# Kernel tuning notes

Measured on AMD Instinct MI355X. Metric: run time of the kernel, lower is better.

## Reference

```python
import jax, jax.numpy as jnp
import numpy as np

N, E, G = 50000, 600000, 128
ND, ED, H, T, L = 32, 16, 128, 128, 4


def setup_inputs() -> dict:
    key = jax.random.key(0)
    ks = jax.random.split(key, 32)
    s = 0.05
    nrm = lambda k, shp: (jax.random.normal(k, shp, jnp.float32) * s)
    inp = {
        'node_f': jax.random.normal(ks[0], (N, ND), jnp.float32),
        'node_x': jax.random.normal(ks[1], (N, 3), jnp.float32),
        'edge_w': jax.random.normal(ks[2], (E, ED), jnp.float32),
        'src': jax.random.randint(ks[3], (E,), 0, N, jnp.int32),
        'dst': jax.random.randint(ks[4], (E,), 0, N, jnp.int32),
        'graph_ids': jnp.sort(jax.random.randint(ks[5], (N,), 0, G, jnp.int32)),
        'W_in': nrm(ks[6], (ND, H)), 'b_in': jnp.zeros((H,), jnp.float32),
        'W_e': nrm(ks[7], (ED, H)), 'b_e': jnp.zeros((H,), jnp.float32),
        'msg_W1': nrm(ks[8], (L, 3 * H + 1, H)), 'msg_b1': jnp.zeros((L, H), jnp.float32),
        'msg_W2': nrm(ks[9], (L, H, H)), 'msg_b2': jnp.zeros((L, H), jnp.float32),
        'upd_W1': nrm(ks[10], (L, H, H)), 'upd_b1': jnp.zeros((L, H), jnp.float32),
        'upd_W2': nrm(ks[11], (L, H, H)), 'upd_b2': jnp.zeros((L, H), jnp.float32),
        'W_out': nrm(ks[12], (2 * H, T)), 'b_out': jnp.zeros((T,), jnp.float32),
    }
    return inp


def reference(node_f, node_x, edge_w, src, dst, graph_ids,
              W_in, b_in, W_e, b_e,
              msg_W1, msg_b1, msg_W2, msg_b2,
              upd_W1, upd_b1, upd_W2, upd_b2,
              W_out, b_out):
    relu = jax.nn.relu
    # input node / edge embeddings
    f = relu(node_f @ W_in + b_in)            # [N, H]
    w = relu(edge_w @ W_e + b_e)              # [E, H]
    # squared distance per edge (positions are static across layers)
    sq = jnp.sum((node_x[src] - node_x[dst]) ** 2, axis=-1, keepdims=True)  # [E, 1]
    for i in range(L):
        mi = jnp.concatenate([f[src], f[dst], w, sq], axis=-1)  # [E, 3H+1]
        m = relu(relu(mi @ msg_W1[i] + msg_b1[i]) @ msg_W2[i] + msg_b2[i])  # [E, H]
        m_sum = jax.ops.segment_sum(m, dst, num_segments=N)     # scatter-sum to dst
        u = m_sum + f
        f = relu(relu(u @ upd_W1[i] + upd_b1[i]) @ upd_W2[i] + upd_b2[i])
    # per-graph mean / max readout
    counts = jax.ops.segment_sum(jnp.ones((N,), f.dtype), graph_ids, num_segments=G)
    mean = jax.ops.segment_sum(f, graph_ids, num_segments=G) / jnp.maximum(counts, 1.0)[:, None]
    mx = jax.ops.segment_max(f, graph_ids, num_segments=G)
    mx = jnp.where(counts[:, None] > 0, mx, 0.0)
    return jnp.concatenate([mean, mx], axis=-1) @ W_out + b_out  # [G, T]
```

## Files before the change

kernel.cpp:

```cpp
#include <hip/hip_runtime.h>
#include <hip/hip_fp16.h>

typedef _Float16 f16;
typedef _Float16 f16x8 __attribute__((ext_vector_type(8)));
typedef float f32x4 __attribute__((ext_vector_type(4)));

#define N_NODES 50000
#define N_EDGES 600000
#define G_GRAPHS 128
#define H 128
#define NP 50176
#define NT_E 18750
#define NB_E 1024
#define NT_N 1563

__global__ void k_f0(const float* __restrict__ node_f, const float* __restrict__ W_in,
                     const float* __restrict__ b_in, f16* __restrict__ fh)
{
    __shared__ float sW[32 * 128];
    __shared__ float sx[8][32];
    const int tid = threadIdx.x;
    const int base = blockIdx.x * 8;
    for (int i = tid; i < 32 * 128; i += 128) sW[i] = W_in[i];
    for (int i = tid; i < 8 * 32; i += 128) {
        int u = i >> 5, k = i & 31;
        int n = base + u;
        sx[u][k] = (n < N_NODES) ? node_f[(size_t)n * 32 + k] : 0.0f;
    }
    __syncthreads();
    const float bj = b_in[tid];
    #pragma unroll
    for (int u = 0; u < 8; ++u) {
        int n = base + u;
        if (n >= N_NODES) break;
        float acc = bj;
        #pragma unroll
        for (int k = 0; k < 32; ++k) acc = fmaf(sx[u][k], sW[k * 128 + tid], acc);
        fh[(size_t)n * H + tid] = (f16)fmaxf(acc, 0.0f);
    }
}

__global__ void k_hist(const int* __restrict__ dst, int* __restrict__ cnt)
{
    int e = blockIdx.x * 256 + threadIdx.x;
    if (e < N_EDGES) atomicAdd(&cnt[dst[e]], 1);
}

__global__ void k_scanA(const int* __restrict__ cnt, int* __restrict__ rowptr,
                        int* __restrict__ bsum)
{
    __shared__ int s[256];
    const int t = threadIdx.x;
    const int i = blockIdx.x * 256 + t;
    int v = cnt[i];
    s[t] = v;
    __syncthreads();
    #pragma unroll
    for (int off = 1; off < 256; off <<= 1) {
        int x = (t >= off) ? s[t - off] : 0;
        __syncthreads();
        s[t] += x;
        __syncthreads();
    }
    rowptr[i] = s[t] - v;
    if (t == 255) bsum[blockIdx.x] = s[255];
}

__global__ void k_scanB(const int* __restrict__ bsum, int* __restrict__ boff)
{
    __shared__ int s[256];
    const int t = threadIdx.x;
    int v = (t < 196) ? bsum[t] : 0;
    s[t] = v;
    __syncthreads();
    #pragma unroll
    for (int off = 1; off < 256; off <<= 1) {
        int x = (t >= off) ? s[t - off] : 0;
        __syncthreads();
        s[t] += x;
        __syncthreads();
    }
    boff[t] = s[t] - v;
}

__global__ void k_scanC(int* __restrict__ rowptr, const int* __restrict__ boff)
{
    int i = blockIdx.x * 256 + threadIdx.x;
    rowptr[i] += boff[blockIdx.x];
}

__global__ void k_scatter_idx(const int* __restrict__ dst, const int* __restrict__ rowptr,
                              int* __restrict__ fill, int* __restrict__ perm_eidx)
{
    int e = blockIdx.x * 256 + threadIdx.x;
    if (e >= N_EDGES) return;
    int d = dst[e];
    int p = rowptr[d] + atomicAdd(&fill[d], 1);
    perm_eidx[p] = e;
}

__global__ void k_gather(const int* __restrict__ perm_eidx, const float* __restrict__ edge_w,
                         const int* __restrict__ src, const int* __restrict__ dst,
                         const float* __restrict__ node_x,
                         int* __restrict__ perm_src, int* __restrict__ perm_dst,
                         float* __restrict__ perm_sq, f16* __restrict__ perm_ewh)
{
    int pp = blockIdx.x * 256 + threadIdx.x;
    if (pp >= N_EDGES) return;
    int e = perm_eidx[pp];
    int s = src[e], d = dst[e];
    float dx = node_x[s * 3 + 0] - node_x[d * 3 + 0];
    float dy = node_x[s * 3 + 1] - node_x[d * 3 + 1];
    float dz = node_x[s * 3 + 2] - node_x[d * 3 + 2];
    perm_src[pp] = s;
    perm_dst[pp] = d;
    perm_sq[pp] = dx * dx + dy * dy + dz * dz;
    const float4* pw = (const float4*)(edge_w + (size_t)e * 16);
    float4 w0 = pw[0], w1 = pw[1], w2 = pw[2], w3 = pw[3];
    f16x8 v0, v1;
    v0[0] = (f16)w0.x; v0[1] = (f16)w0.y; v0[2] = (f16)w0.z; v0[3] = (f16)w0.w;
    v0[4] = (f16)w1.x; v0[5] = (f16)w1.y; v0[6] = (f16)w1.z; v0[7] = (f16)w1.w;
    v1[0] = (f16)w2.x; v1[1] = (f16)w2.y; v1[2] = (f16)w2.z; v1[3] = (f16)w2.w;
    v1[4] = (f16)w3.x; v1[5] = (f16)w3.y; v1[6] = (f16)w3.z; v1[7] = (f16)w3.w;
    f16x8* q = (f16x8*)(perm_ewh + (size_t)pp * 16);
    q[0] = v0; q[1] = v1;
}

__global__ __launch_bounds__(512, 2) void k_edge2(
    const f16* __restrict__ fh,
    const int* __restrict__ perm_src, const int* __restrict__ perm_dst,
    const float* __restrict__ perm_sq, const f16* __restrict__ perm_ewh,
    const float* __restrict__ W_e, const float* __restrict__ b_e,
    const float* __restrict__ W1, const float* __restrict__ b1,
    const float* __restrict__ W2, const float* __restrict__ b2,
    f16* __restrict__ msum)
{
    const int tid = threadIdx.x;
    const int wave = tid >> 6;
    const int lane = tid & 63;
    const int l16 = lane & 15;
    const int lq  = lane >> 4;
    const int col = wave * 16 + l16;

    f16x8 wef, w1f[12], w2f[4];
    #pragma unroll
    for (int j = 0; j < 8; ++j) {
        int k = lq * 8 + j;
        wef[j] = (k < 16) ? (f16)W_e[(size_t)k * H + col] : (f16)0.0f;
    }
    #pragma unroll
    for (int k = 0; k < 12; ++k)
        #pragma unroll
        for (int j = 0; j < 8; ++j)
            w1f[k][j] = (f16)W1[(size_t)(k * 32 + lq * 8 + j) * H + col];
    #pragma unroll
    for (int k = 0; k < 4; ++k)
        #pragma unroll
        for (int j = 0; j < 8; ++j)
            w2f[k][j] = (f16)W2[(size_t)(k * 32 + lq * 8 + j) * H + col];
    const float w1last = W1[(size_t)384 * H + col];
    const float b1v = b1[col], b2v = b2[col], bev = b_e[col];

    __shared__ alignas(16) f16 Atile[32][392];
    __shared__ alignas(16) f16 h1B[2][32][136];
    __shared__ int   s_src[2][32];
    __shared__ int   s_dst[2][32];
    __shared__ float s_sq[2][32];

    const int b = ((blockIdx.x & 7) << 7) | (blockIdx.x >> 3);
    const int t0 = (int)((long)b * NT_E / NB_E);
    const int t1 = (int)((long)(b + 1) * NT_E / NB_E);

    if (tid < 32) {
        int e = t0 * 32 + tid;
        s_src[0][tid] = perm_src[e];
        s_dst[0][tid] = perm_dst[e];
        s_sq[0][tid]  = perm_sq[e];
    }
    __syncthreads();

    int p = 0, q = 0;
    for (int t = t0; t < t1; ++t, p ^= 1, q ^= 1) {
        {
            int row = tid >> 4, ch = tid & 15;
            int j = ((row >> 2) & 3) * 8 + (row >> 4) * 4 + (row & 3);
            int sv = s_src[p][j];
            int dv = s_dst[p][j];
            ((int4*)&Atile[row][0])[ch]   = ((const int4*)(fh + (size_t)sv * H))[ch];
            ((int4*)&Atile[row][128])[ch] = ((const int4*)(fh + (size_t)dv * H))[ch];
        }
        #pragma unroll
        for (int m = 0; m < 2; ++m) {
            f16x8 a;
            if (lq < 2) {
                int j = (l16 >> 2) * 8 + m * 4 + (l16 & 3);
                int e = t * 32 + j;
                a = *(const f16x8*)(perm_ewh + (size_t)e * 16 + lq * 8);
            } else {
                #pragma unroll
                for (int jj = 0; jj < 8; ++jj) a[jj] = (f16)0.0f;
            }
            f32x4 c = {bev, bev, bev, bev};
            c = __builtin_amdgcn_mfma_f32_16x16x32_f16(a, wef, c, 0, 0, 0);
            #pragma unroll
            for (int r = 0; r < 4; ++r)
                Atile[m * 16 + lq * 4 + r][256 + col] = (f16)fmaxf(c[r], 0.0f);
        }
        if (tid < 32 && t + 1 < t1) {
            int e = (t + 1) * 32 + tid;
            s_src[p ^ 1][tid] = perm_src[e];
            s_dst[p ^ 1][tid] = perm_dst[e];
            s_sq[p ^ 1][tid]  = perm_sq[e];
        }
        __syncthreads();

        int dc[8];
        f32x4 acc1[2];
        #pragma unroll
        for (int m = 0; m < 2; ++m)
            #pragma unroll
            for (int r = 0; r < 4; ++r) {
                int j = lq * 8 + m * 4 + r;
                dc[m * 4 + r] = s_dst[p][j];
                acc1[m][r] = fmaf(s_sq[p][j], w1last, b1v);
            }
        #pragma unroll
        for (int k = 0; k < 12; ++k) {
            #pragma unroll
            for (int m = 0; m < 2; ++m) {
                f16x8 a = *(const f16x8*)&Atile[m * 16 + l16][k * 32 + lq * 8];
                acc1[m] = __builtin_amdgcn_mfma_f32_16x16x32_f16(a, w1f[k], acc1[m], 0, 0, 0);
            }
        }
        #pragma unroll
        for (int m = 0; m < 2; ++m)
            #pragma unroll
            for (int r = 0; r < 4; ++r)
                h1B[q][m * 16 + lq * 4 + r][col] = (f16)fmaxf(acc1[m][r], 0.0f);
        __syncthreads();

        f32x4 acc2[2];
        #pragma unroll
        for (int m = 0; m < 2; ++m) {
            f32x4 c = {b2v, b2v, b2v, b2v};
            acc2[m] = c;
        }
        #pragma unroll
        for (int k = 0; k < 4; ++k) {
            #pragma unroll
            for (int m = 0; m < 2; ++m) {
                f16x8 a = *(const f16x8*)&h1B[q][m * 16 + l16][k * 32 + lq * 8];
                acc2[m] = __builtin_amdgcn_mfma_f32_16x16x32_f16(a, w2f[k], acc2[m], 0, 0, 0);
            }
        }
        {
            float run = fmaxf(acc2[0][0], 0.0f);
            int cd = dc[0];
            #pragma unroll
            for (int i = 1; i < 8; ++i) {
                float v = fmaxf(acc2[i >> 2][i & 3], 0.0f);
                int d = dc[i];
                if (d == cd) {
                    run += v;
                } else {
                    float nb = __shfl_xor(run, 1);
                    if ((l16 & 1) == 0) {
                        union { f16 h[2]; __half2 v2; } u;
                        u.h[0] = (f16)run; u.h[1] = (f16)nb;
                        unsafeAtomicAdd((__half2*)&msum[(size_t)cd * H + col], u.v2);
                    }
                    run = v; cd = d;
                }
            }
            float nb = __shfl_xor(run, 1);
            if ((l16 & 1) == 0) {
                union { f16 h[2]; __half2 v2; } u;
                u.h[0] = (f16)run; u.h[1] = (f16)nb;
                unsafeAtomicAdd((__half2*)&msum[(size_t)cd * H + col], u.v2);
            }
        }
    }
}

__global__ __launch_bounds__(256, 4) void k_update(
    const f16* __restrict__ msum, f16* __restrict__ fh,
    const float* __restrict__ W1, const float* __restrict__ b1,
    const float* __restrict__ W2, const float* __restrict__ b2)
{
    const int tid = threadIdx.x;
    const int wave = tid >> 6;
    const int lane = tid & 63;
    const int l16 = lane & 15;
    const int lq = lane >> 4;
    const int colbase = wave * 32;

    f16x8 w1fr[4][2], w2fr[4][2];
    float b1v[2], b2v[2];
    #pragma unroll
    for (int nt = 0; nt < 2; ++nt) {
        const int col = colbase + nt * 16 + l16;
        #pragma unroll
        for (int k = 0; k < 4; ++k) {
            f16x8 v1, v2;
            #pragma unroll
            for (int j = 0; j < 8; ++j) {
                v1[j] = (f16)W1[(size_t)(k * 32 + lq * 8 + j) * H + col];
                v2[j] = (f16)W2[(size_t)(k * 32 + lq * 8 + j) * H + col];
            }
            w1fr[k][nt] = v1;
            w2fr[k][nt] = v2;
        }
        b1v[nt] = b1[col];
        b2v[nt] = b2[col];
    }

    __shared__ alignas(16) f16 U[32][136];
    for (int tile = blockIdx.x; tile < NT_N; tile += gridDim.x) {
        __syncthreads();
        const int n0 = tile * 32;
        {
            int row = tid >> 3, ch = tid & 7;
            int n = n0 + row;
            if (n < N_NODES) {
                const f16x8* pm = (const f16x8*)(msum + (size_t)n * H) + ch * 2;
                const f16x8* pf = (const f16x8*)(fh + (size_t)n * H) + ch * 2;
                f16x8 m0 = pm[0], m1 = pm[1];
                f16x8 f0 = pf[0], f1 = pf[1];
                f16 tmp[16];
                #pragma unroll
                for (int j = 0; j < 8; ++j) {
                    tmp[j]     = (f16)((float)m0[j] + (float)f0[j]);
                    tmp[8 + j] = (f16)((float)m1[j] + (float)f1[j]);
                }
                int4* q0 = (int4*)(&U[row][ch * 16]);
                q0[0] = ((const int4*)tmp)[0];
                q0[1] = ((const int4*)tmp)[1];
            }
        }
        __syncthreads();

        f32x4 acc[2][2];
        #pragma unroll
        for (int m = 0; m < 2; ++m)
            #pragma unroll
            for (int nt = 0; nt < 2; ++nt) {
                f32x4 c = {b1v[nt], b1v[nt], b1v[nt], b1v[nt]};
                acc[m][nt] = c;
            }
        #pragma unroll
        for (int k = 0; k < 4; ++k) {
            #pragma unroll
            for (int m = 0; m < 2; ++m) {
                f16x8 a = *(const f16x8*)&U[m * 16 + l16][k * 32 + lq * 8];
                #pragma unroll
                for (int nt = 0; nt < 2; ++nt)
                    acc[m][nt] = __builtin_amdgcn_mfma_f32_16x16x32_f16(a, w1fr[k][nt], acc[m][nt], 0, 0, 0);
            }
        }
        __syncthreads();
        #pragma unroll
        for (int m = 0; m < 2; ++m)
            #pragma unroll
            for (int nt = 0; nt < 2; ++nt)
                #pragma unroll
                for (int r = 0; r < 4; ++r)
                    U[m * 16 + lq * 4 + r][colbase + nt * 16 + l16] = (f16)fmaxf(acc[m][nt][r], 0.0f);
        __syncthreads();

        f32x4 acc2[2][2];
        #pragma unroll
        for (int m = 0; m < 2; ++m)
            #pragma unroll
            for (int nt = 0; nt < 2; ++nt) {
                f32x4 c = {b2v[nt], b2v[nt], b2v[nt], b2v[nt]};
                acc2[m][nt] = c;
            }
        #pragma unroll
        for (int k = 0; k < 4; ++k) {
            #pragma unroll
            for (int m = 0; m < 2; ++m) {
                f16x8 a = *(const f16x8*)&U[m * 16 + l16][k * 32 + lq * 8];
                #pragma unroll
                for (int nt = 0; nt < 2; ++nt)
                    acc2[m][nt] = __builtin_amdgcn_mfma_f32_16x16x32_f16(a, w2fr[k][nt], acc2[m][nt], 0, 0, 0);
            }
        }
        #pragma unroll
        for (int m = 0; m < 2; ++m)
            #pragma unroll
            for (int nt = 0; nt < 2; ++nt)
                #pragma unroll
                for (int r = 0; r < 4; ++r) {
                    int row = m * 16 + lq * 4 + r;
                    int n = n0 + row;
                    if (n < N_NODES)
                        fh[(size_t)n * H + colbase + nt * 16 + l16] = (f16)fmaxf(acc2[m][nt][r], 0.0f);
                }
    }
}

__global__ void k_readout(const f16* __restrict__ fh, const int* __restrict__ gid,
                          float* __restrict__ gsum, float* __restrict__ gmax,
                          int* __restrict__ gcnt)
{
    __shared__ int s_gid[64];
    const int tid = threadIdx.x;
    const int base = blockIdx.x * 64;
    if (tid < 64) s_gid[tid] = (base + tid < N_NODES) ? gid[base + tid] : -1;
    __syncthreads();
    if (tid < 64 && base + tid < N_NODES) atomicAdd(&gcnt[s_gid[tid]], 1);

    float lsum = 0.0f, lmax = 0.0f;
    int cur = s_gid[0];
    if (cur >= 0) {
        for (int i = 0; i < 64; ++i) {
            int g = s_gid[i];
            if (g < 0) break;
            if (g != cur) {
                unsafeAtomicAdd(&gsum[(size_t)cur * H + tid], lsum);
                atomicMax((int*)&gmax[(size_t)cur * H + tid], __float_as_int(lmax));
                lsum = 0.0f; lmax = 0.0f; cur = g;
            }
            float v = (float)fh[(size_t)(base + i) * H + tid];
            lsum += v;
            lmax = fmaxf(lmax, v);
        }
        unsafeAtomicAdd(&gsum[(size_t)cur * H + tid], lsum);
        atomicMax((int*)&gmax[(size_t)cur * H + tid], __float_as_int(lmax));
    }
}

__global__ void k_out(const float* __restrict__ gsum, const float* __restrict__ gmax,
                      const int* __restrict__ gcnt, const float* __restrict__ W_out,
                      const float* __restrict__ b_out, float* __restrict__ out)
{
    __shared__ float sm[128], sx[128];
    const int g = blockIdx.x, t = threadIdx.x;
    const float inv = 1.0f / fmaxf((float)gcnt[g], 1.0f);
    sm[t] = gsum[(size_t)g * H + t] * inv;
    sx[t] = gmax[(size_t)g * H + t];
    __syncthreads();
    float acc = b_out[t];
    for (int k = 0; k < H; ++k) {
        acc = fmaf(sm[k], W_out[(size_t)k * 128 + t], acc);
        acc = fmaf(sx[k], W_out[(size_t)(128 + k) * 128 + t], acc);
    }
    out[(size_t)g * 128 + t] = acc;
}

extern "C" void kernel_launch(void* const* d_in, const int* in_sizes, int n_in,
                              void* d_out, int out_size, void* d_ws, size_t ws_size,
                              hipStream_t stream)
{
    const float* node_f = (const float*)d_in[0];
    const float* node_x = (const float*)d_in[1];
    const float* edge_w = (const float*)d_in[2];
    const int*   src    = (const int*)d_in[3];
    const int*   dst    = (const int*)d_in[4];
    const int*   gid    = (const int*)d_in[5];
    const float* W_in   = (const float*)d_in[6];
    const float* b_in   = (const float*)d_in[7];
    const float* W_e    = (const float*)d_in[8];
    const float* b_e    = (const float*)d_in[9];
    const float* msg_W1 = (const float*)d_in[10];
    const float* msg_b1 = (const float*)d_in[11];
    const float* msg_W2 = (const float*)d_in[12];
    const float* msg_b2 = (const float*)d_in[13];
    const float* upd_W1 = (const float*)d_in[14];
    const float* upd_b1 = (const float*)d_in[15];
    const float* upd_W2 = (const float*)d_in[16];
    const float* upd_b2 = (const float*)d_in[17];
    const float* W_out  = (const float*)d_in[18];
    const float* b_out  = (const float*)d_in[19];
    float* out = (float*)d_out;

    char* ws = (char*)d_ws;
    size_t off = 0;
    f16*   fh       = (f16*)(ws + off);   off += (size_t)N_NODES * H * 2;
    f16*   perm_ewh = (f16*)(ws + off);   off += (size_t)N_EDGES * 16 * 2;
    int*   perm_src = (int*)(ws + off);   off += (size_t)N_EDGES * 4;
    int*   perm_dst = (int*)(ws + off);   off += (size_t)N_EDGES * 4;
    float* perm_sq  = (float*)(ws + off); off += (size_t)N_EDGES * 4;
    int*   rowptr   = (int*)(ws + off);   off += (size_t)NP * 4;
    int*   cnt      = (int*)(ws + off);   off += (size_t)NP * 4;
    int*   bsum     = (int*)(ws + off);   off += 256 * 4;
    int*   boff     = (int*)(ws + off);   off += 256 * 4;
    f16*   msum     = (f16*)(ws + off);   off += (size_t)N_NODES * H * 2;
    float* gsum     = (float*)(ws + off); off += (size_t)G_GRAPHS * H * 4;
    float* gmax     = (float*)(ws + off); off += (size_t)G_GRAPHS * H * 4;
    int*   gcnt     = (int*)(ws + off);   off += (size_t)G_GRAPHS * 4;
    int*   perm_eidx = (int*)msum;

    k_f0<<<(N_NODES + 7) / 8, 128, 0, stream>>>(node_f, W_in, b_in, fh);

    (void)hipMemsetAsync(cnt, 0, (size_t)NP * 4, stream);
    k_hist<<<(N_EDGES + 255) / 256, 256, 0, stream>>>(dst, cnt);
    k_scanA<<<NP / 256, 256, 0, stream>>>(cnt, rowptr, bsum);
    k_scanB<<<1, 256, 0, stream>>>(bsum, boff);
    k_scanC<<<NP / 256, 256, 0, stream>>>(rowptr, boff);
    (void)hipMemsetAsync(cnt, 0, (size_t)NP * 4, stream);
    k_scatter_idx<<<(N_EDGES + 255) / 256, 256, 0, stream>>>(dst, rowptr, cnt, perm_eidx);
    k_gather<<<(N_EDGES + 255) / 256, 256, 0, stream>>>(perm_eidx, edge_w, src, dst, node_x,
                                                        perm_src, perm_dst, perm_sq, perm_ewh);

    for (int l = 0; l < 4; ++l) {
        (void)hipMemsetAsync(msum, 0, (size_t)N_NODES * H * 2, stream);
        k_edge2<<<NB_E, 512, 0, stream>>>(fh, perm_src, perm_dst, perm_sq, perm_ewh,
                                          W_e, b_e,
                                          msg_W1 + (size_t)l * 385 * H, msg_b1 + (size_t)l * H,
                                          msg_W2 + (size_t)l * H * H,  msg_b2 + (size_t)l * H,
                                          msum);
        k_update<<<512, 256, 0, stream>>>(msum, fh,
                                          upd_W1 + (size_t)l * H * H, upd_b1 + (size_t)l * H,
                                          upd_W2 + (size_t)l * H * H, upd_b2 + (size_t)l * H);
    }

    (void)hipMemsetAsync(gsum, 0, (size_t)G_GRAPHS * H * 4, stream);
    (void)hipMemsetAsync(gmax, 0, (size_t)G_GRAPHS * H * 4, stream);
    (void)hipMemsetAsync(gcnt, 0, (size_t)G_GRAPHS * 4, stream);
    k_readout<<<(N_NODES + 63) / 64, 128, 0, stream>>>(fh, gid, gsum, gmax, gcnt);
    k_out<<<G_GRAPHS, 128, 0, stream>>>(gsum, gmax, gcnt, W_out, b_out, out);
}
```

Baseline: 1.476 ms.

## Software-pipeline gathers in message and update kernels via register prefetch

The message kernel now prefetches the next tile's src/dst feature rows, edge-weight fragments and the index/sq metadata two tiles ahead into registers, writing them into shared memory at the end of the current iteration. This overlaps the global gather latency with the MFMA compute. The update kernel similarly prefetches the next tile's msum and fh rows into registers and uses a separate h1b buffer to drop one barrier, lowering launch_bounds occupancy from 4 to 3 blocks per SM. The cost is higher register pressure and lower occupancy. There is also a possible hazard where the update kernel prefetches fh rows of a later tile while other blocks are writing fh, though those rows differ.

```diff
diff --git a/kernel.cpp b/kernel.cpp
--- a/kernel.cpp
+++ b/kernel.cpp
@@ -171,6 +171,9 @@
     const int t0 = (int)((long)b * NT_E / NB_E);
     const int t1 = (int)((long)(b + 1) * NT_E / NB_E);
 
+    const int srow = tid >> 4, sch = tid & 15;
+    const int sj = ((srow >> 2) & 3) * 8 + ((srow >> 4) << 2) + (srow & 3);
+
     if (tid < 32) {
         int e = t0 * 32 + tid;
         s_src[0][tid] = perm_src[e];
@@ -178,24 +181,35 @@
         s_sq[0][tid]  = perm_sq[e];
     }
     __syncthreads();
-
-    int p = 0, q = 0;
-    for (int t = t0; t < t1; ++t, p ^= 1, q ^= 1) {
-        {
-            int row = tid >> 4, ch = tid & 15;
-            int j = ((row >> 2) & 3) * 8 + (row >> 4) * 4 + (row & 3);
-            int sv = s_src[p][j];
-            int dv = s_dst[p][j];
-            ((int4*)&Atile[row][0])[ch]   = ((const int4*)(fh + (size_t)sv * H))[ch];
-            ((int4*)&Atile[row][128])[ch] = ((const int4*)(fh + (size_t)dv * H))[ch];
-        }
+    int4 rs_, rd_;
+    {
+        int sv = s_src[0][sj], dv = s_dst[0][sj];
+        rs_ = ((const int4*)(fh + (size_t)sv * H))[sch];
+        rd_ = ((const int4*)(fh + (size_t)dv * H))[sch];
+    }
+    f16x8 rew[2];
+    #pragma unroll
+    for (int m = 0; m < 2; ++m) {
+        if (lq < 2) {
+            int j = (l16 >> 2) * 8 + m * 4 + (l16 & 3);
+            rew[m] = *(const f16x8*)(perm_ewh + (size_t)(t0 * 32 + j) * 16 + lq * 8);
+        }
+    }
+    int mr_s = 0, mr_d = 0; float mr_q = 0.0f;
+    if (tid < 32) {
+        int e = min((t0 + 1) * 32 + tid, N_EDGES - 1);
+        mr_s = perm_src[e]; mr_d = perm_dst[e]; mr_q = perm_sq[e];
+    }
+    ((int4*)&Atile[srow][0])[sch]   = rs_;
+    ((int4*)&Atile[srow][128])[sch] = rd_;
+
+    int P = 0, Q = 0;
+    for (int t = t0; t < t1; ++t, P ^= 1, Q ^= 1) {
         #pragma unroll
         for (int m = 0; m < 2; ++m) {
             f16x8 a;
             if (lq < 2) {
-                int j = (l16 >> 2) * 8 + m * 4 + (l16 & 3);
-                int e = t * 32 + j;
-                a = *(const f16x8*)(perm_ewh + (size_t)e * 16 + lq * 8);
+                a = rew[m];
             } else {
                 #pragma unroll
                 for (int jj = 0; jj < 8; ++jj) a[jj] = (f16)0.0f;
@@ -206,11 +220,10 @@
             for (int r = 0; r < 4; ++r)
                 Atile[m * 16 + lq * 4 + r][256 + col] = (f16)fmaxf(c[r], 0.0f);
         }
-        if (tid < 32 && t + 1 < t1) {
-            int e = (t + 1) * 32 + tid;
-            s_src[p ^ 1][tid] = perm_src[e];
-            s_dst[p ^ 1][tid] = perm_dst[e];
-            s_sq[p ^ 1][tid]  = perm_sq[e];
+        if (tid < 32) {
+            s_src[P ^ 1][tid] = mr_s;
+            s_dst[P ^ 1][tid] = mr_d;
+            s_sq[P ^ 1][tid]  = mr_q;
         }
         __syncthreads();
 
@@ -221,9 +234,25 @@
             #pragma unroll
             for (int r = 0; r < 4; ++r) {
                 int j = lq * 8 + m * 4 + r;
-                dc[m * 4 + r] = s_dst[p][j];
-                acc1[m][r] = fmaf(s_sq[p][j], w1last, b1v);
-            }
+                dc[m * 4 + r] = s_dst[P][j];
+                acc1[m][r] = fmaf(s_sq[P][j], w1last, b1v);
+            }
+        if (t + 1 < t1) {
+            int sv = s_src[P ^ 1][sj], dv = s_dst[P ^ 1][sj];
+            rs_ = ((const int4*)(fh + (size_t)sv * H))[sch];
+            rd_ = ((const int4*)(fh + (size_t)dv * H))[sch];
+            #pragma unroll
+            for (int m = 0; m < 2; ++m) {
+                if (lq < 2) {
+                    int j = (l16 >> 2) * 8 + m * 4 + (l16 & 3);
+                    rew[m] = *(const f16x8*)(perm_ewh + (size_t)((t + 1) * 32 + j) * 16 + lq * 8);
+                }
+            }
+        }
+        if (tid < 32) {
+            int e = min((t + 2) * 32 + tid, N_EDGES - 1);
+            mr_s = perm_src[e]; mr_d = perm_dst[e]; mr_q = perm_sq[e];
+        }
         #pragma unroll
         for (int k = 0; k < 12; ++k) {
             #pragma unroll
@@ -236,7 +265,7 @@
         for (int m = 0; m < 2; ++m)
             #pragma unroll
             for (int r = 0; r < 4; ++r)
-                h1B[q][m * 16 + lq * 4 + r][col] = (f16)fmaxf(acc1[m][r], 0.0f);
+                h1B[Q][m * 16 + lq * 4 + r][col] = (f16)fmaxf(acc1[m][r], 0.0f);
         __syncthreads();
 
         f32x4 acc2[2];
@@ -249,7 +278,7 @@
         for (int k = 0; k < 4; ++k) {
             #pragma unroll
             for (int m = 0; m < 2; ++m) {
-                f16x8 a = *(const f16x8*)&h1B[q][m * 16 + l16][k * 32 + lq * 8];
+                f16x8 a = *(const f16x8*)&h1B[Q][m * 16 + l16][k * 32 + lq * 8];
                 acc2[m] = __builtin_amdgcn_mfma_f32_16x16x32_f16(a, w2f[k], acc2[m], 0, 0, 0);
             }
         }
@@ -279,10 +308,14 @@
                 unsafeAtomicAdd((__half2*)&msum[(size_t)cd * H + col], u.v2);
             }
         }
-    }
-}
-
-__global__ __launch_bounds__(256, 4) void k_update(
+        if (t + 1 < t1) {
+            ((int4*)&Atile[srow][0])[sch]   = rs_;
+            ((int4*)&Atile[srow][128])[sch] = rd_;
+        }
+    }
+}
+
+__global__ __launch_bounds__(256, 3) void k_update(
     const f16* __restrict__ msum, f16* __restrict__ fh,
     const float* __restrict__ W1, const float* __restrict__ b1,
     const float* __restrict__ W2, const float* __restrict__ b2)
@@ -315,26 +348,37 @@
     }
 
     __shared__ alignas(16) f16 U[32][136];
-    for (int tile = blockIdx.x; tile < NT_N; tile += gridDim.x) {
-        __syncthreads();
+    __shared__ alignas(16) f16 h1b[32][136];
+    const int row = tid >> 3, ch = tid & 7;
+
+    int tile = blockIdx.x;
+    f16x8 rm0, rm1, rf0, rf1;
+    if (tile < NT_N) {
+        int n = min(tile * 32 + row, N_NODES - 1);
+        const f16x8* pm = (const f16x8*)(msum + (size_t)n * H) + ch * 2;
+        const f16x8* pf = (const f16x8*)(fh + (size_t)n * H) + ch * 2;
+        rm0 = pm[0]; rm1 = pm[1]; rf0 = pf[0]; rf1 = pf[1];
+    }
+    for (; tile < NT_N; tile += gridDim.x) {
         const int n0 = tile * 32;
         {
-            int row = tid >> 3, ch = tid & 7;
-            int n = n0 + row;
-            if (n < N_NODES) {
+            f16 tmp[16];
+            #pragma unroll
+            for (int j = 0; j < 8; ++j) {
+                tmp[j]     = (f16)((float)rm0[j] + (float)rf0[j]);
+                tmp[8 + j] = (f16)((float)rm1[j] + (float)rf1[j]);
+            }
+            int4* q0 = (int4*)(&U[row][ch * 16]);
+            q0[0] = ((const int4*)tmp)[0];
+            q0[1] = ((const int4*)tmp)[1];
+        }
+        {
+            int nt_ = tile + gridDim.x;
+            if (nt_ < NT_N) {
+                int n = min(nt_ * 32 + row, N_NODES - 1);
                 const f16x8* pm = (const f16x8*)(msum + (size_t)n * H) + ch * 2;
                 const f16x8* pf = (const f16x8*)(fh + (size_t)n * H) + ch * 2;
-                f16x8 m0 = pm[0], m1 = pm[1];
-                f16x8 f0 = pf[0], f1 = pf[1];
-                f16 tmp[16];
-                #pragma unroll
-                for (int j = 0; j < 8; ++j) {
-                    tmp[j]     = (f16)((float)m0[j] + (float)f0[j]);
-                    tmp[8 + j] = (f16)((float)m1[j] + (float)f1[j]);
-                }
-                int4* q0 = (int4*)(&U[row][ch * 16]);
-                q0[0] = ((const int4*)tmp)[0];
-                q0[1] = ((const int4*)tmp)[1];
+                rm0 = pm[0]; rm1 = pm[1]; rf0 = pf[0]; rf1 = pf[1];
             }
         }
         __syncthreads();
@@ -357,14 +401,13 @@
                     acc[m][nt] = __builtin_amdgcn_mfma_f32_16x16x32_f16(a, w1fr[k][nt], acc[m][nt], 0, 0, 0);
             }
         }
-        __syncthreads();
         #pragma unroll
         for (int m = 0; m < 2; ++m)
             #pragma unroll
             for (int nt = 0; nt < 2; ++nt)
                 #pragma unroll
                 for (int r = 0; r < 4; ++r)
-                    U[m * 16 + lq * 4 + r][colbase + nt * 16 + l16] = (f16)fmaxf(acc[m][nt][r], 0.0f);
+                    h1b[m * 16 + lq * 4 + r][colbase + nt * 16 + l16] = (f16)fmaxf(acc[m][nt][r], 0.0f);
         __syncthreads();
 
         f32x4 acc2[2][2];
@@ -379,7 +422,7 @@
         for (int k = 0; k < 4; ++k) {
             #pragma unroll
             for (int m = 0; m < 2; ++m) {
-                f16x8 a = *(const f16x8*)&U[m * 16 + l16][k * 32 + lq * 8];
+                f16x8 a = *(const f16x8*)&h1b[m * 16 + l16][k * 32 + lq * 8];
                 #pragma unroll
                 for (int nt = 0; nt < 2; ++nt)
                     acc2[m][nt] = __builtin_amdgcn_mfma_f32_16x16x32_f16(a, w2fr[k][nt], acc2[m][nt], 0, 0, 0);
@@ -391,8 +434,8 @@
             for (int nt = 0; nt < 2; ++nt)
                 #pragma unroll
                 for (int r = 0; r < 4; ++r) {
-                    int row = m * 16 + lq * 4 + r;
-                    int n = n0 + row;
+                    int rr = m * 16 + lq * 4 + r;
+                    int n = n0 + rr;
                     if (n < N_NODES)
                         fh[(size_t)n * H + colbase + nt * 16 + l16] = (f16)fmaxf(acc2[m][nt][r], 0.0f);
                 }
```

After: 1.288 ms. 12.8% less time.
